# Kernel tuning notes

Hardware: AMD Instinct MI355X
Metric: run time of the kernel (lower is better)

The kernel has to match this reference:

```python
import jax, jax.numpy as jnp
import numpy as np

NX, NY = 128, 128
NT = 50
DECAY = 0.1
M1 = M2 = 12
WIDTH = 64


def _spectral(x, w1, w2):
    # x: [B, W, NX, NY]; w1/w2: complex [W, W, M1, M2]
    xf = jnp.fft.rfft2(x)                                   # [B, W, NX, NY//2+1]
    of = jnp.zeros(xf.shape[:2] + (NX, NY // 2 + 1), jnp.complex64)
    of = of.at[:, :, :M1, :M2].set(jnp.einsum('bixy,ioxy->boxy', xf[:, :, :M1, :M2], w1))
    of = of.at[:, :, NX - M1:, :M2].set(jnp.einsum('bixy,ioxy->boxy', xf[:, :, NX - M1:, :M2], w2))
    return jnp.fft.irfft2(of, s=(NX, NY))


def _forward(xyt_q, obs_coords, obs_vals, x_grid, y_grid,
             fc0_w, fc0_b, spec_w1r, spec_w1i, spec_w2r, spec_w2i,
             pw_w, pw_b, fc1_w, fc1_b, fc2_w, fc2_b,
             nb_idx, sensor_iy, sensor_ix, Lx, Ly):
    B, K = nb_idx.shape
    # ---- gather obs, temporal-decay weight, scatter-add into sparse grid ----
    sensor_ids = nb_idx // NT                               # [B, K]
    t_nb = obs_coords[nb_idx, 2]                            # [B, K]
    w = jnp.exp(-DECAY * jnp.abs(t_nb - xyt_q[:, None, 2])) # [B, K]
    vals = obs_vals[nb_idx] * w                             # [B, K]
    lin = sensor_iy[sensor_ids] * NY + sensor_ix[sensor_ids]
    flat = (lin + jnp.arange(B)[:, None] * (NX * NY)).ravel()
    sparse = jnp.zeros(B * NX * NY, obs_vals.dtype).at[flat].add(vals.ravel())
    counts = jnp.zeros(B * NX * NY, obs_vals.dtype).at[flat].add(w.ravel())
    grid = jnp.where(counts > 0, sparse / jnp.maximum(counts, 1e-6), 0.0).reshape(B, NX, NY)
    # ---- FNO core ----
    inp = jnp.stack([grid,
                     jnp.broadcast_to(x_grid, (B, NX, NY)),
                     jnp.broadcast_to(y_grid, (B, NX, NY))], axis=1)  # [B, 3, NX, NY]
    x = jnp.einsum('bcxy,cw->bwxy', inp, fc0_w) + fc0_b[None, :, None, None]
    for i in range(4):
        y = (_spectral(x, spec_w1r[i] + 1j * spec_w1i[i], spec_w2r[i] + 1j * spec_w2i[i])
             + jnp.einsum('bcxy,oc->boxy', x, pw_w[i]) + pw_b[i][None, :, None, None])
        x = jax.nn.gelu(y, approximate=False) if i < 3 else y
    h = jax.nn.gelu(jnp.einsum('bwxy,wf->bxyf', x, fc1_w) + fc1_b, approximate=False)
    field = (jnp.einsum('bxyf,fo->bxyo', h, fc2_w) + fc2_b).transpose(0, 3, 1, 2)  # [B, 3, NX, NY]
    # ---- bilinear sample at query points ----
    x01 = jnp.clip(xyt_q[:, 0] / max(Lx, 1e-6), 0.0, 1.0)
    y01 = jnp.clip(xyt_q[:, 1] / max(Ly, 1e-6), 0.0, 1.0)
    gx = x01 * (NX - 1)
    gy = y01 * (NY - 1)
    x0 = jnp.floor(gx).astype(jnp.int32)
    y0 = jnp.floor(gy).astype(jnp.int32)
    x1 = jnp.minimum(x0 + 1, NX - 1)
    y1 = jnp.minimum(y0 + 1, NY - 1)
    wx = (gx - x0)[:, None]
    wy = (gy - y0)[:, None]
    b = jnp.arange(B)
    f00 = field[b, :, x0, y0]
    f10 = field[b, :, x1, y0]
    f01 = field[b, :, x0, y1]
    f11 = field[b, :, x1, y1]
    top = f00 * (1.0 - wx) + f10 * wx
    bot = f01 * (1.0 - wx) + f11 * wx
    return top * (1.0 - wy) + bot * wy                       # [B, 3]


def setup_inputs() -> dict:
    key = jax.random.key(0)
    ks = jax.random.split(key, 20)
    B, K, NOBS, NS = 64, 64, 50000, 1000
    scale = 1.0 / (WIDTH * WIDTH)
    inp = {
        'xyt_q': jax.random.uniform(ks[0], (B, 3), jnp.float32),
        'obs_coords': jax.random.uniform(ks[1], (NOBS, 3), jnp.float32),
        'obs_vals': jax.random.normal(ks[2], (NOBS,), jnp.float32),
        'x_grid': jax.random.uniform(ks[3], (NX, NY), jnp.float32),
        'y_grid': jax.random.uniform(ks[4], (NX, NY), jnp.float32),
        'fc0_w': jax.random.normal(ks[5], (3, WIDTH), jnp.float32) * 0.3,
        'fc0_b': jnp.zeros((WIDTH,), jnp.float32),
        'spec_w1r': scale * jax.random.uniform(ks[6], (4, WIDTH, WIDTH, M1, M2), jnp.float32),
        'spec_w1i': scale * jax.random.uniform(ks[7], (4, WIDTH, WIDTH, M1, M2), jnp.float32),
        'spec_w2r': scale * jax.random.uniform(ks[8], (4, WIDTH, WIDTH, M1, M2), jnp.float32),
        'spec_w2i': scale * jax.random.uniform(ks[9], (4, WIDTH, WIDTH, M1, M2), jnp.float32),
        'pw_w': jax.random.normal(ks[10], (4, WIDTH, WIDTH), jnp.float32) * (1.0 / np.sqrt(WIDTH)),
        'pw_b': jnp.zeros((4, WIDTH), jnp.float32),
        'fc1_w': jax.random.normal(ks[11], (WIDTH, 128), jnp.float32) * (1.0 / np.sqrt(WIDTH)),
        'fc1_b': jnp.zeros((128,), jnp.float32),
        'fc2_w': jax.random.normal(ks[12], (128, 3), jnp.float32) * (1.0 / np.sqrt(128.0)),
        'fc2_b': jnp.zeros((3,), jnp.float32),
        'nb_idx': jax.random.randint(ks[13], (B, K), 0, NOBS, jnp.int32),
        'sensor_iy': jax.random.randint(ks[14], (NS,), 0, NX, jnp.int32),
        'sensor_ix': jax.random.randint(ks[15], (NS,), 0, NY, jnp.int32),
        'Lx': 1,
        'Ly': 1,
    }
    return inp


def reference(xyt_q, obs_coords, obs_vals, x_grid, y_grid,
              fc0_w, fc0_b, spec_w1r, spec_w1i, spec_w2r, spec_w2i,
              pw_w, pw_b, fc1_w, fc1_b, fc2_w, fc2_b,
              nb_idx, sensor_iy, sensor_ix, Lx, Ly):
    return _forward(xyt_q, obs_coords, obs_vals, x_grid, y_grid,
                    fc0_w, fc0_b, spec_w1r, spec_w1i, spec_w2r, spec_w2i,
                    pw_w, pw_b, fc1_w, fc1_b, fc2_w, fc2_b,
                    nb_idx, sensor_iy, sensor_ix, Lx, Ly)
```

## Files before the change

kernel.cpp:

```cpp
#include <hip/hip_runtime.h>
#include <math.h>

#define NXg 128
#define NYg 128
#define Pg  (NXg*NYg)
#define Bq  64
#define Wd  64
#define NKX 24
#define NMODE (NKX*12)
#define PI2_128 0.04908738521234052f

typedef _Float16 f16x8 __attribute__((ext_vector_type(8)));
typedef _Float16 f16x4 __attribute__((ext_vector_type(4)));
typedef float    f32x4 __attribute__((ext_vector_type(4)));

#define OFF_TC  0
#define OFF_TS  (OFF_TC + 128)
#define F32_END (OFF_TS + 128)
#define H_T1E  0
#define H_T1ET (H_T1E + 32*128)
#define H_A2   (H_T1ET + 128*32)
#define H_PWH  (H_A2 + 48*256)
#define H_T2ET (H_PWH + 4*64*64)
#define H_XFHR (H_T2ET + 128*64)
#define H_XFHI (H_XFHR + 288*4096)
#define H_OFHR (H_XFHI + 288*4096)
#define H_OFHI (H_OFHR + 288*4096)
#define H_WHR  (H_OFHI + 288*4096)
#define H_WHI  (H_WHR + (size_t)4*288*4096)
#define H_YG   (H_WHI + (size_t)4*288*4096)
#define H_X    (H_YG + (size_t)Bq*Wd*128*24)
#define H_U    (H_X + (size_t)Bq*128*128*64)

__device__ __forceinline__ float fast_gelu(float v) {
    float a = fabsf(v) * 0.70710678118654752f;
    float t = 1.f / (1.f + 0.3275911f * a);
    float p = t * (0.254829592f + t * (-0.284496736f + t * (1.421413741f +
              t * (-1.453152027f + t * 1.061405429f))));
    float er = 1.f - p * __expf(-a * a);
    er = copysignf(er, v);
    return 0.5f * v * (1.f + er);
}

__global__ void k_prep(_Float16* T1e_g, _Float16* T1eT_g, _Float16* A2_g,
                       const float* pww, _Float16* PWh, _Float16* T2eT_g,
                       float* Tc, float* Ts,
                       const float* xyt, const float* obs_c, const float* obs_v,
                       const int* nb, const int* siy, const int* six,
                       float* val, float* cnt,
                       const float* w1r, const float* w1i,
                       const float* w2r, const float* w2i,
                       _Float16* Whr, _Float16* Whi) {
    __shared__ _Float16 L[64][146];
    int blk = blockIdx.x;
    if (blk < 64) {
        int t = blk * 256 + threadIdx.x;
        if (t < 32*128) {
            int r = t >> 7, y = t & 127;
            float v = 0.f;
            if (r < 12)      v =  cosf((float)((r * y) & 127) * PI2_128);
            else if (r < 24) v = -sinf((float)(((r-12) * y) & 127) * PI2_128);
            T1e_g[t] = (_Float16)v;
            int y2 = t >> 5, r2 = t & 31;
            float v2 = 0.f;
            if (r2 < 12)      v2 =  cosf((float)((r2 * y2) & 127) * PI2_128);
            else if (r2 < 24) v2 = -sinf((float)(((r2-12) * y2) & 127) * PI2_128);
            T1eT_g[t] = (_Float16)v2;
        }
        if (t < 48*256) {
            int m = t >> 8, k = t & 255;
            int x = k & 127;
            int hi = (k >= 128);
            float v;
            if (m < 24) {
                int kx = (m < 12) ? m : (104 + m);
                float th = (float)((kx * x) & 127) * PI2_128;
                v = hi ? sinf(th) : cosf(th);
            } else {
                int mm = m - 24;
                int kx = (mm < 12) ? mm : (104 + mm);
                float th = (float)((kx * x) & 127) * PI2_128;
                v = hi ? cosf(th) : -sinf(th);
            }
            A2_g[t] = (_Float16)v;
        }
        if (t < 4*64*64) PWh[t] = (_Float16)pww[t];
        if (t < 128*64) {
            int x = t >> 6, k = t & 63;
            float v = 0.f;
            if (k < 24) {
                int kx = (k < 12) ? k : (104 + k);
                v = cosf((float)((kx * x) & 127) * PI2_128);
            } else if (k < 48) {
                int kk = k - 24;
                int kx = (kk < 12) ? kk : (104 + kk);
                v = sinf((float)((kx * x) & 127) * PI2_128);
            }
            T2eT_g[t] = (_Float16)v;
        }
        if (t < 128) {
            float th = (float)t * PI2_128;
            Tc[t] = cosf(th);
            Ts[t] = sinf(th);
        }
    } else if (blk < 80) {
        int t = (blk - 64) * 256 + threadIdx.x;
        int b = t >> 6;
        int id = nb[t];
        int sid = id / 50;
        float tq = xyt[b*3 + 2];
        float w = expf(-0.1f * fabsf(obs_c[id*3 + 2] - tq));
        int lin = siy[sid] * NYg + six[sid];
        atomicAdd(&val[b*Pg + lin], obs_v[id] * w);
        atomicAdd(&cnt[b*Pg + lin], w);
    } else {
        int u = blk - 80;
        int layer = u >> 8;
        int rem = u & 255;
        int o = rem & 63, ri = (rem >> 6) & 1, half = rem >> 7;
        const float* src = half ? (ri ? w2i : w2r) : (ri ? w1i : w1r);
        _Float16* dst = ri ? Whi : Whr;
        size_t sbase = (size_t)layer * 589824 + (size_t)o * 144;
        for (int idx = threadIdx.x; idx < 9216; idx += 256) {
            int i = idx / 144, m = idx - i*144;
            L[i][m] = (_Float16)src[sbase + (size_t)i*9216 + m];
        }
        __syncthreads();
        size_t obase = ((size_t)(layer*288 + half*144) << 12) + o*64;
        for (int idx = threadIdx.x; idx < 9216; idx += 256) {
            int m = idx >> 6, i = idx & 63;
            dst[obase + ((size_t)m << 12) + i] = L[i][m];
        }
    }
}

__device__ __forceinline__ void stageA_bf(const _Float16* __restrict__ T1e_g, int lane, f16x8* bf) {
    int l15 = lane & 15, quad = lane >> 4;
    #pragma unroll
    for (int u = 0; u < 8; u++) {
        int nt2 = u >> 2, q = u & 3;
        bf[u] = *(const f16x8*)&T1e_g[(nt2*16 + l15)*128 + q*32 + quad*8];
    }
}

__device__ __forceinline__ void stageA_core(const _Float16 (*Xn)[76], const f16x8* bf,
                                            _Float16* __restrict__ Yg, int b, int row, int tid) {
    int wave = tid >> 6, lane = tid & 63;
    int l15 = lane & 15, quad = lane >> 4;
    f16x8 af[4];
    #pragma unroll
    for (int q = 0; q < 4; q++)
        #pragma unroll
        for (int j = 0; j < 8; j++)
            af[q][j] = Xn[q*32 + quad*8 + j][wave*16 + l15];
    _Float16* yrow = Yg + (size_t)(b*128 + row) * 1536;
    #pragma unroll
    for (int nt2 = 0; nt2 < 2; nt2++) {
        f32x4 acc = {0.f,0.f,0.f,0.f};
        #pragma unroll
        for (int q = 0; q < 4; q++)
            acc = __builtin_amdgcn_mfma_f32_16x16x32_f16(af[q], bf[nt2*4 + q], acc, 0, 0, 0);
        int t = nt2*16 + l15;
        if (t < 24) {
            #pragma unroll
            for (int r = 0; r < 4; r++)
                yrow[(wave*16 + quad*4 + r)*24 + t] = (_Float16)acc[r];
        }
    }
}

__device__ __forceinline__ void stageA(const _Float16 (*Xn)[76], const _Float16* __restrict__ T1e_g,
                                       _Float16* __restrict__ Yg, int b, int row, int tid) {
    f16x8 bf[8];
    stageA_bf(T1e_g, tid & 63, bf);
    stageA_core(Xn, bf, Yg, b, row, tid);
}

__global__ __launch_bounds__(256) void k_fc0y(const float* __restrict__ val, const float* __restrict__ cnt,
                      const float* __restrict__ xg, const float* __restrict__ yg,
                      const float* __restrict__ w, const float* __restrict__ bb,
                      const _Float16* __restrict__ T1e_g,
                      _Float16* __restrict__ Yg) {
    __shared__ _Float16 Xn[128][76];
    __shared__ float wl[4][64];
    int row = blockIdx.x, b = blockIdx.y;
    int tid = threadIdx.x;
    if (tid < 64) {
        wl[0][tid] = w[tid]; wl[1][tid] = w[64+tid]; wl[2][tid] = w[128+tid]; wl[3][tid] = bb[tid];
    }
    __syncthreads();
    {
        int y = tid & 127, half = tid >> 7;
        int p = row*128 + y;
        float c = cnt[(size_t)b*Pg + p];
        float g = (c > 0.f) ? val[(size_t)b*Pg + p] / fmaxf(c, 1e-6f) : 0.f;
        float a1 = xg[p], a2 = yg[p];
        #pragma unroll
        for (int blk = 0; blk < 4; blk++) {
            f16x8 pk;
            #pragma unroll
            for (int j = 0; j < 8; j++) {
                int o = half*32 + blk*8 + j;
                pk[j] = (_Float16)(g*wl[0][o] + a1*wl[1][o] + a2*wl[2][o] + wl[3][o]);
            }
            *(f16x8*)&Xn[y][half*32 + blk*8] = pk;
        }
    }
    __syncthreads();
    stageA(Xn, T1e_g, Yg, b, row, tid);
}

__global__ __launch_bounds__(256) void k_sB(const _Float16* __restrict__ Yg,
                    const _Float16* __restrict__ A2_g,
                    _Float16* __restrict__ xfhr, _Float16* __restrict__ xfhi) {
    __shared__ _Float16 Ys[4][28][136];
    int bc4 = blockIdx.x << 2;
    int tid = threadIdx.x;
    int wave = tid >> 6, lane = tid & 63;
    int l15 = lane & 15, quad = lane >> 4;
    int b = bc4 >> 6, c0 = bc4 & 63;
    const _Float16* base = Yg + ((size_t)b*128*64 + c0)*24;
    for (int i = tid; i < 1536; i += 256) {
        int x = i / 12, w = i - x*12;
        f16x8 v = *(const f16x8*)&base[(size_t)x*1536 + w*8];
        int e = w*8;
        #pragma unroll
        for (int j = 0; j < 8; j++) {
            int tt = e + j;
            int s = tt / 24, t = tt - s*24;
            Ys[s][t][x] = v[j];
        }
    }
    __syncthreads();
    int bc = bc4 + wave;
    #pragma unroll
    for (int mt = 0; mt < 3; mt++) {
        f32x4 acc = {0.f,0.f,0.f,0.f};
        #pragma unroll
        for (int q = 0; q < 8; q++) {
            f16x8 a = *(const f16x8*)&A2_g[(size_t)(mt*16 + l15)*256 + q*32 + quad*8];
            const _Float16* brow = (q < 4) ? &Ys[wave][l15][q*32 + quad*8]
                                           : &Ys[wave][12 + l15][(q-4)*32 + quad*8];
            f16x8 bfr = *(const f16x8*)brow;
            acc = __builtin_amdgcn_mfma_f32_16x16x32_f16(a, bfr, acc, 0, 0, 0);
        }
        if (l15 < 12) {
            #pragma unroll
            for (int r = 0; r < 4; r++) {
                int m = mt*16 + quad*4 + r;
                if (m < 24) xfhr[(size_t)(m*12 + l15)*4096 + bc] = (_Float16)acc[r];
                else        xfhi[(size_t)((m-24)*12 + l15)*4096 + bc] = (_Float16)acc[r];
            }
        }
    }
}

__global__ __launch_bounds__(256) void k_s3m(const _Float16* __restrict__ xfhr, const _Float16* __restrict__ xfhi,
                    const _Float16* __restrict__ Whr, const _Float16* __restrict__ Whi,
                    _Float16* __restrict__ ofhr, _Float16* __restrict__ ofhi, int layer) {
    __shared__ _Float16 Xr[16][72], Xi[16][72];
    int mode = blockIdx.x;
    int bo = blockIdx.y << 4;
    int tid = threadIdx.x;
    int wave = tid >> 6, lane = tid & 63;
    int l15 = lane & 15, quad = lane >> 4;
    const _Float16* pr = xfhr + (size_t)mode * 4096 + bo*64;
    const _Float16* pi = xfhi + (size_t)mode * 4096 + bo*64;
    if (tid < 128) {
        int b = tid >> 3, seg = tid & 7;
        *(f16x8*)&Xr[b][seg*8] = *(const f16x8*)&pr[tid*8];
        *(f16x8*)&Xi[b][seg*8] = *(const f16x8*)&pi[tid*8];
    }
    __syncthreads();
    size_t wb = ((size_t)(layer*288 + mode)*64 + wave*16 + l15) * 64 + quad*8;
    f16x8 wr0 = *(const f16x8*)&Whr[wb];
    f16x8 wr1 = *(const f16x8*)&Whr[wb + 32];
    f16x8 wi0 = *(const f16x8*)&Whi[wb];
    f16x8 wi1 = *(const f16x8*)&Whi[wb + 32];
    f16x8 xr0 = *(const f16x8*)&Xr[l15][quad*8];
    f16x8 xr1 = *(const f16x8*)&Xr[l15][32 + quad*8];
    f16x8 xi0 = *(const f16x8*)&Xi[l15][quad*8];
    f16x8 xi1 = *(const f16x8*)&Xi[l15][32 + quad*8];
    f16x8 xn0, xn1;
    #pragma unroll
    for (int j = 0; j < 8; j++) { xn0[j] = -xi0[j]; xn1[j] = -xi1[j]; }
    f32x4 cr = {0.f,0.f,0.f,0.f}, ci = {0.f,0.f,0.f,0.f};
    cr = __builtin_amdgcn_mfma_f32_16x16x32_f16(xr0, wr0, cr, 0, 0, 0);
    cr = __builtin_amdgcn_mfma_f32_16x16x32_f16(xr1, wr1, cr, 0, 0, 0);
    cr = __builtin_amdgcn_mfma_f32_16x16x32_f16(xn0, wi0, cr, 0, 0, 0);
    cr = __builtin_amdgcn_mfma_f32_16x16x32_f16(xn1, wi1, cr, 0, 0, 0);
    ci = __builtin_amdgcn_mfma_f32_16x16x32_f16(xr0, wi0, ci, 0, 0, 0);
    ci = __builtin_amdgcn_mfma_f32_16x16x32_f16(xr1, wi1, ci, 0, 0, 0);
    ci = __builtin_amdgcn_mfma_f32_16x16x32_f16(xi0, wr0, ci, 0, 0, 0);
    ci = __builtin_amdgcn_mfma_f32_16x16x32_f16(xi1, wr1, ci, 0, 0, 0);
    #pragma unroll
    for (int r = 0; r < 4; r++) {
        int b = bo + quad*4 + r;
        int o = wave*16 + l15;
        ofhr[(size_t)mode*4096 + b*64 + o] = (_Float16)cr[r];
        ofhi[(size_t)mode*4096 + b*64 + o] = (_Float16)ci[r];
    }
}

__global__ __launch_bounds__(256) void k_sG(const _Float16* __restrict__ ofhr, const _Float16* __restrict__ ofhi,
                    const _Float16* __restrict__ T2eT_g, _Float16* __restrict__ Gh) {
    __shared__ _Float16 As[64][72];
    __shared__ _Float16 Cs[128][72];
    int b = blockIdx.x, t = blockIdx.y;
    int tid = threadIdx.x;
    int wave = tid >> 6, lane = tid & 63;
    int l15 = lane & 15, quad = lane >> 4;
    int ky = (t < 12) ? t : (t - 12);
    float sc = ((ky == 0) ? 1.f : 2.f) * (1.f/16384.f);
    bool isReal = (t < 12);
    if (tid < 192) {
        int kxi = tid >> 3, seg = tid & 7;
        size_t idx = (size_t)(kxi*12 + ky)*4096 + b*64 + seg*8;
        f16x8 vr8 = *(const f16x8*)&ofhr[idx];
        f16x8 vi8 = *(const f16x8*)&ofhi[idx];
        #pragma unroll
        for (int j = 0; j < 8; j++) {
            int o = seg*8 + j;
            float vr = (float)vr8[j] * sc, vi = (float)vi8[j] * sc;
            As[o][kxi]      = (_Float16)(isReal ? vr : vi);
            As[o][24 + kxi] = (_Float16)(isReal ? -vi : vr);
        }
    }
    for (int i = tid; i < 1024; i += 256)
        As[i >> 4][48 + (i & 15)] = (_Float16)0.f;
    __syncthreads();
    f16x8 a0 = *(const f16x8*)&As[wave*16 + l15][quad*8];
    f16x8 a1 = *(const f16x8*)&As[wave*16 + l15][32 + quad*8];
    #pragma unroll
    for (int nt = 0; nt < 8; nt++) {
        f16x8 b0 = *(const f16x8*)&T2eT_g[(nt*16 + l15)*64 + quad*8];
        f16x8 b1 = *(const f16x8*)&T2eT_g[(nt*16 + l15)*64 + 32 + quad*8];
        f32x4 acc = {0.f,0.f,0.f,0.f};
        acc = __builtin_amdgcn_mfma_f32_16x16x32_f16(a0, b0, acc, 0, 0, 0);
        acc = __builtin_amdgcn_mfma_f32_16x16x32_f16(a1, b1, acc, 0, 0, 0);
        f16x4 pk;
        #pragma unroll
        for (int r = 0; r < 4; r++) pk[r] = (_Float16)acc[r];
        *(f16x4*)&Cs[nt*16 + l15][wave*16 + quad*4] = pk;
    }
    __syncthreads();
    float4* o4 = (float4*)Gh;
    for (int i = tid; i < 1024; i += 256) {
        int x = i >> 3, seg = i & 7;
        o4[((size_t)((b*128 + x)*24 + t))*8 + seg] = *(const float4*)&Cs[x][seg*8];
    }
}

__global__ __launch_bounds__(256, 4) void k_s45(_Float16* __restrict__ xh,
                    const _Float16* __restrict__ Gh,
                    const _Float16* __restrict__ T1e_g, const _Float16* __restrict__ T1eT_g,
                    const _Float16* __restrict__ PWh,
                    const float* __restrict__ pwb,
                    _Float16* __restrict__ Yg, int layer,
                    const float* __restrict__ xyt, const int* __restrict__ Lx,
                    const float* __restrict__ val, const float* __restrict__ cnt,
                    const float* __restrict__ xg, const float* __restrict__ yg,
                    const float* __restrict__ fc0w, const float* __restrict__ fc0b) {
    __shared__ _Float16 BsT[2][128][76];
    __shared__ float wl[4][64];
    int rp = blockIdx.x, b = blockIdx.y;
    int row0 = rp << 1;
    int tid = threadIdx.x;
    int wave = tid >> 6, lane = tid & 63;
    int l15 = lane & 15, quad = lane >> 4;

    f16x8 af2[2];
    #pragma unroll
    for (int r2 = 0; r2 < 2; r2++)
        #pragma unroll
        for (int j = 0; j < 8; j++) af2[r2][j] = (_Float16)0.f;
    if (quad < 3) {
        #pragma unroll
        for (int r2 = 0; r2 < 2; r2++) {
            const _Float16* gt = Gh + (size_t)(b*128 + row0 + r2) * 1536 + wave*16 + l15;
            #pragma unroll
            for (int j = 0; j < 8; j++) af2[r2][j] = gt[(quad*8 + j) * 64];
        }
    }

    f16x8 af0 = *(const f16x8*)&PWh[(size_t)(layer*64 + wave*16 + l15)*64 + quad*8];
    f16x8 af1 = *(const f16x8*)&PWh[(size_t)(layer*64 + wave*16 + l15)*64 + 32 + quad*8];
    f16x8 b2a[8];
    #pragma unroll
    for (int nt = 0; nt < 8; nt++)
        b2a[nt] = *(const f16x8*)&T1eT_g[(nt*16 + l15)*32 + quad*8];
    float pb[4];
    #pragma unroll
    for (int r = 0; r < 4; r++)
        pb[r] = pwb[layer*64 + wave*16 + quad*4 + r];

    if (layer == 0) {
        if (tid < 64) {
            wl[0][tid] = fc0w[tid]; wl[1][tid] = fc0w[64+tid];
            wl[2][tid] = fc0w[128+tid]; wl[3][tid] = fc0b[tid];
        }
        __syncthreads();
        int y = tid & 127, half = tid >> 7;
        #pragma unroll
        for (int r2 = 0; r2 < 2; r2++) {
            int p = (row0 + r2)*128 + y;
            float c = cnt[(size_t)b*Pg + p];
            float g = (c > 0.f) ? val[(size_t)b*Pg + p] / fmaxf(c, 1e-6f) : 0.f;
            float a1 = xg[p], a2 = yg[p];
            #pragma unroll
            for (int blk = 0; blk < 4; blk++) {
                f16x8 pkk;
                #pragma unroll
                for (int j = 0; j < 8; j++) {
                    int o = half*32 + blk*8 + j;
                    pkk[j] = (_Float16)(g*wl[0][o] + a1*wl[1][o] + a2*wl[2][o] + wl[3][o]);
                }
                *(f16x8*)&BsT[r2][y][half*32 + blk*8] = pkk;
            }
        }
    } else {
        for (int i = tid; i < 2048; i += 256) {
            int r2 = i >> 10, k = i & 1023;
            int y = k >> 3, seg = k & 7;
            *(float4*)&BsT[r2][y][seg*8] =
                ((const float4*)(xh + (size_t)(b*128 + row0 + r2) * 8192))[k];
        }
    }
    __syncthreads();

    f16x4 pk[2][8];
    #pragma unroll
    for (int r2 = 0; r2 < 2; r2++) {
        f32x4 acc[8];
        #pragma unroll
        for (int nt = 0; nt < 8; nt++) {
            f32x4 a = {0.f,0.f,0.f,0.f};
            f16x8 b0 = *(const f16x8*)&BsT[r2][nt*16 + l15][quad*8];
            f16x8 b1 = *(const f16x8*)&BsT[r2][nt*16 + l15][32 + quad*8];
            a = __builtin_amdgcn_mfma_f32_16x16x32_f16(af0, b0, a, 0, 0, 0);
            a = __builtin_amdgcn_mfma_f32_16x16x32_f16(af1, b1, a, 0, 0, 0);
            a = __builtin_amdgcn_mfma_f32_16x16x32_f16(af2[r2], b2a[nt], a, 0, 0, 0);
            acc[nt] = a;
        }
        #pragma unroll
        for (int nt = 0; nt < 8; nt++)
            #pragma unroll
            for (int r = 0; r < 4; r++)
                pk[r2][nt][r] = (_Float16)fast_gelu(acc[nt][r] + pb[r]);
    }
    __syncthreads();

    #pragma unroll
    for (int r2 = 0; r2 < 2; r2++)
        #pragma unroll
        for (int nt = 0; nt < 8; nt++)
            *(f16x4*)&BsT[r2][nt*16 + l15][wave*16 + quad*4] = pk[r2][nt];
    __syncthreads();

    bool st0 = true, st1 = true;
    if (layer == 2) {
        float Lxf = fmaxf((float)Lx[0], 1e-6f);
        float x01 = fminf(fmaxf(xyt[b*3 + 0] / Lxf, 0.f), 1.f);
        float gxp = x01 * (NXg - 1);
        int x0 = (int)floorf(gxp);
        int x1 = min(x0 + 1, NXg - 1);
        st0 = (row0 == x0) || (row0 == x1);
        st1 = (row0 + 1 == x0) || (row0 + 1 == x1);
    }
    for (int i = tid; i < 2048; i += 256) {
        int r2 = i >> 10, k = i & 1023;
        if (r2 ? st1 : st0) {
            int y = k >> 3, seg = k & 7;
            ((float4*)(xh + (size_t)(b*128 + row0 + r2) * 8192))[k] =
                *(const float4*)&BsT[r2][y][seg*8];
        }
    }

    f16x8 bf[8];
    stageA_bf(T1e_g, lane, bf);
    stageA_core(BsT[0], bf, Yg, b, row0, tid);
    stageA_core(BsT[1], bf, Yg, b, row0 + 1, tid);
}

__global__ __launch_bounds__(256) void k_final(const _Float16* __restrict__ x,
                    const _Float16* __restrict__ ofhr, const _Float16* __restrict__ ofhi,
                    const float* __restrict__ pw, const float* __restrict__ pwb,
                    const float* __restrict__ fc1w, const float* __restrict__ fc1b,
                    const float* __restrict__ fc2w, const float* __restrict__ fc2b,
                    const float* __restrict__ xyt, const int* __restrict__ Lx, const int* __restrict__ Ly,
                    const float* __restrict__ Tc, const float* __restrict__ Ts,
                    float* __restrict__ out) {
    __shared__ float y4[4][64];
    __shared__ float hh[4][129];
    __shared__ int   pxy[4][2];
    __shared__ float wxy[2];
    __shared__ float tc[128], ts[128];
    int b = blockIdx.x;
    if (threadIdx.x < 128) {
        tc[threadIdx.x] = Tc[threadIdx.x];
        ts[threadIdx.x] = Ts[threadIdx.x];
    }
    if (threadIdx.x == 0) {
        float Lxf = fmaxf((float)Lx[0], 1e-6f);
        float Lyf = fmaxf((float)Ly[0], 1e-6f);
        float x01 = fminf(fmaxf(xyt[b*3 + 0] / Lxf, 0.f), 1.f);
        float y01 = fminf(fmaxf(xyt[b*3 + 1] / Lyf, 0.f), 1.f);
        float gx = x01 * (NXg - 1), gy = y01 * (NYg - 1);
        int x0 = (int)floorf(gx), y0 = (int)floorf(gy);
        int x1 = min(x0 + 1, NXg - 1), y1 = min(y0 + 1, NYg - 1);
        wxy[0] = gx - (float)x0;
        wxy[1] = gy - (float)y0;
        pxy[0][0] = x0; pxy[0][1] = y0;
        pxy[1][0] = x1; pxy[1][1] = y0;
        pxy[2][0] = x0; pxy[2][1] = y1;
        pxy[3][0] = x1; pxy[3][1] = y1;
    }
    __syncthreads();
    {
        int p = threadIdx.x >> 6, o = threadIdx.x & 63;
        int px = pxy[p][0], py = pxy[p][1];
        float gkr[12], gki[12];
        #pragma unroll
        for (int ky = 0; ky < 12; ky++) { gkr[ky] = 0.f; gki[ky] = 0.f; }
        for (int kxi = 0; kxi < 24; kxi++) {
            int kx = (kxi < 12) ? kxi : (104 + kxi);
            int m = (kx * px) & 127;
            float cc = tc[m], ss = ts[m];
            #pragma unroll
            for (int ky = 0; ky < 12; ky++) {
                size_t idx = (size_t)(kxi*12 + ky)*4096 + b*64 + o;
                float a = (float)ofhr[idx], bb = (float)ofhi[idx];
                gkr[ky] += a*cc - bb*ss;
                gki[ky] += a*ss + bb*cc;
            }
        }
        float sp = gkr[0];
        #pragma unroll
        for (int ky = 1; ky < 12; ky++) {
            int m = (ky * py) & 127;
            sp += 2.f * (gkr[ky]*tc[m] - gki[ky]*ts[m]);
        }
        float s = 0.f;
        const _Float16* xb = x + ((size_t)(b*128 + px)*128 + py)*64;
        #pragma unroll 4
        for (int c = 0; c < 64; c++)
            s += pw[3*4096 + o*64 + c] * (float)xb[c];
        y4[p][o] = sp * (1.f/16384.f) + s + pwb[3*64 + o];
    }
    __syncthreads();
    for (int i = threadIdx.x; i < 512; i += 256) {
        int p = i >> 7, f = i & 127;
        float s = fc1b[f];
        #pragma unroll 4
        for (int w = 0; w < 64; w++) s += y4[p][w] * fc1w[w*128 + f];
        hh[p][f] = 0.5f * s * (1.f + erff(s * 0.70710678118654752f));
    }
    __syncthreads();
    if (threadIdx.x < 3) {
        int o3 = threadIdx.x;
        float f4[4];
        #pragma unroll
        for (int p = 0; p < 4; p++) {
            float s = fc2b[o3];
            #pragma unroll 4
            for (int f = 0; f < 128; f++) s += hh[p][f] * fc2w[f*3 + o3];
            f4[p] = s;
        }
        float wx = wxy[0], wy = wxy[1];
        float top = f4[0]*(1.f - wx) + f4[1]*wx;
        float bot = f4[2]*(1.f - wx) + f4[3]*wx;
        out[b*3 + o3] = top*(1.f - wy) + bot*wy;
    }
}

extern "C" void kernel_launch(void* const* d_in, const int* in_sizes, int n_in,
                              void* d_out, int out_size, void* d_ws, size_t ws_size,
                              hipStream_t stream) {
    const float* xyt    = (const float*)d_in[0];
    const float* obs_c  = (const float*)d_in[1];
    const float* obs_v  = (const float*)d_in[2];
    const float* xg     = (const float*)d_in[3];
    const float* yg     = (const float*)d_in[4];
    const float* fc0w   = (const float*)d_in[5];
    const float* fc0b   = (const float*)d_in[6];
    const float* w1r    = (const float*)d_in[7];
    const float* w1i    = (const float*)d_in[8];
    const float* w2r    = (const float*)d_in[9];
    const float* w2i    = (const float*)d_in[10];
    const float* pww    = (const float*)d_in[11];
    const float* pwb    = (const float*)d_in[12];
    const float* fc1w   = (const float*)d_in[13];
    const float* fc1b   = (const float*)d_in[14];
    const float* fc2w   = (const float*)d_in[15];
    const float* fc2b   = (const float*)d_in[16];
    const int*   nb     = (const int*)d_in[17];
    const int*   siy    = (const int*)d_in[18];
    const int*   six    = (const int*)d_in[19];
    const int*   Lx     = (const int*)d_in[20];
    const int*   Ly     = (const int*)d_in[21];
    float* out = (float*)d_out;

    float* W = (float*)d_ws;
    float* Tc  = W + OFF_TC;
    float* Ts  = W + OFF_TS;
    _Float16* Hbase = (_Float16*)(W + F32_END);
    _Float16* T1e_g  = Hbase + H_T1E;
    _Float16* T1eT_g = Hbase + H_T1ET;
    _Float16* A2_g   = Hbase + H_A2;
    _Float16* PWh    = Hbase + H_PWH;
    _Float16* T2eT_g = Hbase + H_T2ET;
    _Float16* xfhr   = Hbase + H_XFHR;
    _Float16* xfhi   = Hbase + H_XFHI;
    _Float16* ofhr   = Hbase + H_OFHR;
    _Float16* ofhi   = Hbase + H_OFHI;
    _Float16* Whr    = Hbase + H_WHR;
    _Float16* Whi    = Hbase + H_WHI;
    _Float16* Yg     = Hbase + H_YG;
    _Float16* xh     = Hbase + H_X;
    float*    val    = (float*)(Hbase + H_U);
    float*    cnt    = val + Bq*Pg;
    _Float16* Gh2    = Hbase + H_U + (size_t)4*Bq*Pg;

    hipMemsetAsync(val, 0, (size_t)2 * Bq * Pg * sizeof(float), stream);

    k_prep<<<1104, 256, 0, stream>>>(T1e_g, T1eT_g, A2_g, pww, PWh, T2eT_g, Tc, Ts,
                                     xyt, obs_c, obs_v, nb, siy, six, val, cnt,
                                     w1r, w1i, w2r, w2i, Whr, Whi);
    k_fc0y<<<dim3(128, Bq), 256, 0, stream>>>(val, cnt, xg, yg, fc0w, fc0b, T1e_g, Yg);

    for (int l = 0; l < 3; l++) {
        k_sB<<<Bq*Wd/4, 256, 0, stream>>>(Yg, A2_g, xfhr, xfhi);
        k_s3m<<<dim3(288, 4), 256, 0, stream>>>(xfhr, xfhi, Whr, Whi, ofhr, ofhi, l);
        k_sG<<<dim3(Bq, 24), 256, 0, stream>>>(ofhr, ofhi, T2eT_g, Gh2);
        k_s45<<<dim3(64, Bq), 256, 0, stream>>>(xh, Gh2, T1e_g, T1eT_g, PWh, pwb, Yg, l,
                                                xyt, Lx, val, cnt, xg, yg, fc0w, fc0b);
    }
    k_sB<<<Bq*Wd/4, 256, 0, stream>>>(Yg, A2_g, xfhr, xfhi);
    k_s3m<<<dim3(288, 4), 256, 0, stream>>>(xfhr, xfhi, Whr, Whi, ofhr, ofhi, 3);
    k_final<<<Bq, 256, 0, stream>>>(xh, ofhr, ofhi, pww, pwb, fc1w, fc1b, fc2w, fc2b,
                                    xyt, Lx, Ly, Tc, Ts, out);
}
```

Measured before the change: 613.5 us.

## Double k_s45 block size so each half of the block handles one row

k_s45 now launches 512 threads per block instead of 256. Each group of four waves processes one of the two grid rows, so the two-row loops in the pointwise/GELU MFMA stage and the stage-A DFT projection become a per-wave computation, with stageA_core inlined per row. This cuts the serial work per wave and the register pressure from the two-row arrays, giving more parallel waves for latency hiding. In exchange, blocks are larger and launch bounds assume up to 8 blocks per CU.

Result: slower. 806.4 us (+31.4%).

```diff
diff --git a/kernel.cpp b/kernel.cpp
--- a/kernel.cpp
+++ b/kernel.cpp
@@ -351,7 +351,7 @@
     }
 }
 
-__global__ __launch_bounds__(256, 4) void k_s45(_Float16* __restrict__ xh,
+__global__ __launch_bounds__(512, 8) void k_s45(_Float16* __restrict__ xh,
                     const _Float16* __restrict__ Gh,
                     const _Float16* __restrict__ T1e_g, const _Float16* __restrict__ T1eT_g,
                     const _Float16* __restrict__ PWh,
@@ -366,25 +366,23 @@
     int rp = blockIdx.x, b = blockIdx.y;
     int row0 = rp << 1;
     int tid = threadIdx.x;
-    int wave = tid >> 6, lane = tid & 63;
+    int w4 = (tid >> 6) & 3;
+    int r2 = tid >> 8;
+    int lane = tid & 63;
     int l15 = lane & 15, quad = lane >> 4;
-
-    f16x8 af2[2];
-    #pragma unroll
-    for (int r2 = 0; r2 < 2; r2++)
-        #pragma unroll
-        for (int j = 0; j < 8; j++) af2[r2][j] = (_Float16)0.f;
+    int row = row0 + r2;
+
+    f16x8 af2;
+    #pragma unroll
+    for (int j = 0; j < 8; j++) af2[j] = (_Float16)0.f;
     if (quad < 3) {
-        #pragma unroll
-        for (int r2 = 0; r2 < 2; r2++) {
-            const _Float16* gt = Gh + (size_t)(b*128 + row0 + r2) * 1536 + wave*16 + l15;
-            #pragma unroll
-            for (int j = 0; j < 8; j++) af2[r2][j] = gt[(quad*8 + j) * 64];
-        }
-    }
-
-    f16x8 af0 = *(const f16x8*)&PWh[(size_t)(layer*64 + wave*16 + l15)*64 + quad*8];
-    f16x8 af1 = *(const f16x8*)&PWh[(size_t)(layer*64 + wave*16 + l15)*64 + 32 + quad*8];
+        const _Float16* gt = Gh + (size_t)(b*128 + row) * 1536 + w4*16 + l15;
+        #pragma unroll
+        for (int j = 0; j < 8; j++) af2[j] = gt[(quad*8 + j) * 64];
+    }
+
+    f16x8 af0 = *(const f16x8*)&PWh[(size_t)(layer*64 + w4*16 + l15)*64 + quad*8];
+    f16x8 af1 = *(const f16x8*)&PWh[(size_t)(layer*64 + w4*16 + l15)*64 + 32 + quad*8];
     f16x8 b2a[8];
     #pragma unroll
     for (int nt = 0; nt < 8; nt++)
@@ -392,7 +390,7 @@
     float pb[4];
     #pragma unroll
     for (int r = 0; r < 4; r++)
-        pb[r] = pwb[layer*64 + wave*16 + quad*4 + r];
+        pb[r] = pwb[layer*64 + w4*16 + quad*4 + r];
 
     if (layer == 0) {
         if (tid < 64) {
@@ -400,61 +398,53 @@
             wl[2][tid] = fc0w[128+tid]; wl[3][tid] = fc0b[tid];
         }
         __syncthreads();
-        int y = tid & 127, half = tid >> 7;
-        #pragma unroll
-        for (int r2 = 0; r2 < 2; r2++) {
-            int p = (row0 + r2)*128 + y;
-            float c = cnt[(size_t)b*Pg + p];
-            float g = (c > 0.f) ? val[(size_t)b*Pg + p] / fmaxf(c, 1e-6f) : 0.f;
-            float a1 = xg[p], a2 = yg[p];
+        int y = tid & 127, half = (tid >> 7) & 1;
+        int p = row*128 + y;
+        float c = cnt[(size_t)b*Pg + p];
+        float g = (c > 0.f) ? val[(size_t)b*Pg + p] / fmaxf(c, 1e-6f) : 0.f;
+        float a1 = xg[p], a2 = yg[p];
+        #pragma unroll
+        for (int blk = 0; blk < 4; blk++) {
+            f16x8 pkk;
             #pragma unroll
-            for (int blk = 0; blk < 4; blk++) {
-                f16x8 pkk;
-                #pragma unroll
-                for (int j = 0; j < 8; j++) {
-                    int o = half*32 + blk*8 + j;
-                    pkk[j] = (_Float16)(g*wl[0][o] + a1*wl[1][o] + a2*wl[2][o] + wl[3][o]);
-                }
-                *(f16x8*)&BsT[r2][y][half*32 + blk*8] = pkk;
+            for (int j = 0; j < 8; j++) {
+                int o = half*32 + blk*8 + j;
+                pkk[j] = (_Float16)(g*wl[0][o] + a1*wl[1][o] + a2*wl[2][o] + wl[3][o]);
             }
+            *(f16x8*)&BsT[r2][y][half*32 + blk*8] = pkk;
         }
     } else {
-        for (int i = tid; i < 2048; i += 256) {
-            int r2 = i >> 10, k = i & 1023;
+        for (int i = tid; i < 2048; i += 512) {
+            int rr = i >> 10, k = i & 1023;
             int y = k >> 3, seg = k & 7;
-            *(float4*)&BsT[r2][y][seg*8] =
-                ((const float4*)(xh + (size_t)(b*128 + row0 + r2) * 8192))[k];
-        }
-    }
-    __syncthreads();
-
-    f16x4 pk[2][8];
-    #pragma unroll
-    for (int r2 = 0; r2 < 2; r2++) {
-        f32x4 acc[8];
-        #pragma unroll
-        for (int nt = 0; nt < 8; nt++) {
-            f32x4 a = {0.f,0.f,0.f,0.f};
-            f16x8 b0 = *(const f16x8*)&BsT[r2][nt*16 + l15][quad*8];
-            f16x8 b1 = *(const f16x8*)&BsT[r2][nt*16 + l15][32 + quad*8];
-            a = __builtin_amdgcn_mfma_f32_16x16x32_f16(af0, b0, a, 0, 0, 0);
-            a = __builtin_amdgcn_mfma_f32_16x16x32_f16(af1, b1, a, 0, 0, 0);
-            a = __builtin_amdgcn_mfma_f32_16x16x32_f16(af2[r2], b2a[nt], a, 0, 0, 0);
-            acc[nt] = a;
-        }
-        #pragma unroll
-        for (int nt = 0; nt < 8; nt++)
-            #pragma unroll
-            for (int r = 0; r < 4; r++)
-                pk[r2][nt][r] = (_Float16)fast_gelu(acc[nt][r] + pb[r]);
-    }
-    __syncthreads();
-
-    #pragma unroll
-    for (int r2 = 0; r2 < 2; r2++)
-        #pragma unroll
-        for (int nt = 0; nt < 8; nt++)
-            *(f16x4*)&BsT[r2][nt*16 + l15][wave*16 + quad*4] = pk[r2][nt];
+            *(float4*)&BsT[rr][y][seg*8] =
+                ((const float4*)(xh + (size_t)(b*128 + row0 + rr) * 8192))[k];
+        }
+    }
+    __syncthreads();
+
+    f32x4 acc[8];
+    #pragma unroll
+    for (int nt = 0; nt < 8; nt++) {
+        f32x4 a = {0.f,0.f,0.f,0.f};
+        f16x8 b0 = *(const f16x8*)&BsT[r2][nt*16 + l15][quad*8];
+        f16x8 b1 = *(const f16x8*)&BsT[r2][nt*16 + l15][32 + quad*8];
+        a = __builtin_amdgcn_mfma_f32_16x16x32_f16(af0, b0, a, 0, 0, 0);
+        a = __builtin_amdgcn_mfma_f32_16x16x32_f16(af1, b1, a, 0, 0, 0);
+        a = __builtin_amdgcn_mfma_f32_16x16x32_f16(af2, b2a[nt], a, 0, 0, 0);
+        acc[nt] = a;
+    }
+    f16x4 pk[8];
+    #pragma unroll
+    for (int nt = 0; nt < 8; nt++)
+        #pragma unroll
+        for (int r = 0; r < 4; r++)
+            pk[nt][r] = (_Float16)fast_gelu(acc[nt][r] + pb[r]);
+    __syncthreads();
+
+    #pragma unroll
+    for (int nt = 0; nt < 8; nt++)
+        *(f16x4*)&BsT[r2][nt*16 + l15][w4*16 + quad*4] = pk[nt];
     __syncthreads();
 
     bool st0 = true, st1 = true;
@@ -467,19 +457,37 @@
         st0 = (row0 == x0) || (row0 == x1);
         st1 = (row0 + 1 == x0) || (row0 + 1 == x1);
     }
-    for (int i = tid; i < 2048; i += 256) {
-        int r2 = i >> 10, k = i & 1023;
-        if (r2 ? st1 : st0) {
+    for (int i = tid; i < 2048; i += 512) {
+        int rr = i >> 10, k = i & 1023;
+        if (rr ? st1 : st0) {
             int y = k >> 3, seg = k & 7;
-            ((float4*)(xh + (size_t)(b*128 + row0 + r2) * 8192))[k] =
-                *(const float4*)&BsT[r2][y][seg*8];
+            ((float4*)(xh + (size_t)(b*128 + row0 + rr) * 8192))[k] =
+                *(const float4*)&BsT[rr][y][seg*8];
         }
     }
 
     f16x8 bf[8];
     stageA_bf(T1e_g, lane, bf);
-    stageA_core(BsT[0], bf, Yg, b, row0, tid);
-    stageA_core(BsT[1], bf, Yg, b, row0 + 1, tid);
+    f16x8 af[4];
+    #pragma unroll
+    for (int q = 0; q < 4; q++)
+        #pragma unroll
+        for (int j = 0; j < 8; j++)
+            af[q][j] = BsT[r2][q*32 + quad*8 + j][w4*16 + l15];
+    _Float16* yrow = Yg + (size_t)(b*128 + row) * 1536;
+    #pragma unroll
+    for (int nt2 = 0; nt2 < 2; nt2++) {
+        f32x4 a = {0.f,0.f,0.f,0.f};
+        #pragma unroll
+        for (int q = 0; q < 4; q++)
+            a = __builtin_amdgcn_mfma_f32_16x16x32_f16(af[q], bf[nt2*4 + q], a, 0, 0, 0);
+        int t = nt2*16 + l15;
+        if (t < 24) {
+            #pragma unroll
+            for (int r = 0; r < 4; r++)
+                yrow[(w4*16 + quad*4 + r)*24 + t] = (_Float16)a[r];
+        }
+    }
 }
 
 __global__ __launch_bounds__(256) void k_final(const _Float16* __restrict__ x,
@@ -632,7 +640,7 @@
         k_sB<<<Bq*Wd/4, 256, 0, stream>>>(Yg, A2_g, xfhr, xfhi);
         k_s3m<<<dim3(288, 4), 256, 0, stream>>>(xfhr, xfhi, Whr, Whi, ofhr, ofhi, l);
         k_sG<<<dim3(Bq, 24), 256, 0, stream>>>(ofhr, ofhi, T2eT_g, Gh2);
-        k_s45<<<dim3(64, Bq), 256, 0, stream>>>(xh, Gh2, T1e_g, T1eT_g, PWh, pwb, Yg, l,
+        k_s45<<<dim3(64, Bq), 512, 0, stream>>>(xh, Gh2, T1e_g, T1eT_g, PWh, pwb, Yg, l,
                                                 xyt, Lx, val, cnt, xg, yg, fc0w, fc0b);
     }
     k_sB<<<Bq*Wd/4, 256, 0, stream>>>(Yg, A2_g, xfhr, xfhi);
```
